# Performance work log

Hardware: AMD Instinct MI355X
Metric: run time of the kernel (lower is better)

## Reference

```python
import jax, jax.numpy as jnp
import numpy as np

DIM = 256
HEADS = 8
WS = 7  # window_size
EPS = 1e-5


def dwconv1d(x, w, b):
    # x: (B, Cg, L); w: (Cg, 1, k); depthwise (groups=Cg), 'same' padding for odd k
    k = w.shape[-1]
    p = k // 2
    y = jax.lax.conv_general_dilated(
        x, w, window_strides=(1,), padding=[(p, p)],
        dimension_numbers=('NCH', 'OIH', 'NCH'),
        feature_group_count=x.shape[1])
    return y + b[None, :, None]


def group_norm(x, scale, bias, groups):
    # x: (B, C, *spatial); normalize over (C//groups, *spatial) per group
    B, C = x.shape[0], x.shape[1]
    xg = x.reshape(B, groups, -1)
    mean = xg.mean(-1, keepdims=True)
    var = xg.var(-1, keepdims=True)
    xn = ((xg - mean) * jax.lax.rsqrt(var + EPS)).reshape(x.shape)
    bshape = (1, C) + (1,) * (x.ndim - 2)
    return xn * scale.reshape(bshape) + bias.reshape(bshape)


def setup_inputs() -> dict:
    key = jax.random.key(0)
    ks = jax.random.split(key, 16)
    gc = DIM // 4
    d = {"x": jax.random.normal(ks[0], (32, DIM, 56, 56), dtype=jnp.float32)}
    for i, k in enumerate([3, 5, 7, 9]):
        d[f"w_dwc{k}"] = jax.random.normal(ks[1 + i], (gc, 1, k), dtype=jnp.float32) * (1.0 / np.sqrt(k))
        d[f"b_dwc{k}"] = jax.random.normal(ks[5 + i], (gc,), dtype=jnp.float32) * 0.02
    d["norm_h_scale"] = jnp.ones((DIM,), jnp.float32)
    d["norm_h_bias"] = jnp.zeros((DIM,), jnp.float32)
    d["norm_w_scale"] = jnp.ones((DIM,), jnp.float32)
    d["norm_w_bias"] = jnp.zeros((DIM,), jnp.float32)
    d["norm_scale"] = jnp.ones((DIM,), jnp.float32)
    d["norm_bias"] = jnp.zeros((DIM,), jnp.float32)
    d["q_w"] = jax.random.normal(ks[9], (DIM,), dtype=jnp.float32)
    d["k_w"] = jax.random.normal(ks[10], (DIM,), dtype=jnp.float32)
    d["v_w"] = jax.random.normal(ks[11], (DIM,), dtype=jnp.float32)
    return d


def reference(x, w_dwc3, b_dwc3, w_dwc5, b_dwc5, w_dwc7, b_dwc7, w_dwc9, b_dwc9,
              norm_h_scale, norm_h_bias, norm_w_scale, norm_w_bias,
              norm_scale, norm_bias, q_w, k_w, v_w):
    b, c, h, w = x.shape
    head_dim = c // HEADS

    def sa_branch(xm, scale, bias):
        # xm: (B, C, L) -> sigmoid(GroupNorm4(concat of 4 depthwise convs))
        p0, p1, p2, p3 = jnp.split(xm, 4, axis=1)
        y = jnp.concatenate([
            dwconv1d(p0, w_dwc3, b_dwc3),
            dwconv1d(p1, w_dwc5, b_dwc5),
            dwconv1d(p2, w_dwc7, b_dwc7),
            dwconv1d(p3, w_dwc9, b_dwc9)], axis=1)
        return jax.nn.sigmoid(group_norm(y, scale, bias, 4))

    x_h_attn = sa_branch(x.mean(axis=3), norm_h_scale, norm_h_bias)[:, :, :, None]  # (B,C,H,1)
    x_w_attn = sa_branch(x.mean(axis=2), norm_w_scale, norm_w_bias)[:, :, None, :]  # (B,C,1,W)
    xg = x * x_h_attn * x_w_attn

    # AvgPool2d(WS, stride=WS)
    hs, ws_ = h // WS, w // WS
    y = xg.reshape(b, c, hs, WS, ws_, WS).mean(axis=(3, 5))  # (B,C,hs,ws)
    y = group_norm(y, norm_scale, norm_bias, 1)

    n = hs * ws_
    q = (y * q_w[None, :, None, None]).reshape(b, HEADS, head_dim, n)
    k = (y * k_w[None, :, None, None]).reshape(b, HEADS, head_dim, n)
    v = (y * v_w[None, :, None, None]).reshape(b, HEADS, head_dim, n)

    attn = jnp.einsum('bhdn,bhen->bhde', q, k) * (head_dim ** -0.5)
    attn = jax.nn.softmax(attn, axis=-1)
    out = jnp.einsum('bhde,bhen->bhdn', attn, v)  # (B,H,hd,n)

    ca = jax.nn.sigmoid(out.reshape(b, c, n).mean(axis=-1))[:, :, None, None]  # (B,C,1,1)
    return ca * xg
```

## Files before the change

kernel.cpp:

```cpp
#include <hip/hip_runtime.h>
#include <cstdint>
#include <cstddef>

#define NB 32
#define NC 256
#define HW 56
#define PLANE (HW*HW)
#define NPLANE (NB*NC)
#define NHEADS 8
#define HDIM 32
#define NPOOL 64
#define EPSV 1e-5f

__global__ __launch_bounds__(256) void k_means(const float* __restrict__ x,
                                               float* __restrict__ hm,
                                               float* __restrict__ wm) {
    int plane = blockIdx.x;
    __shared__ float sm[PLANE];
    const float4* xp = (const float4*)(x + (size_t)plane * PLANE);
    float4* smp = (float4*)sm;
    int t = threadIdx.x;
    for (int f = t; f < PLANE / 4; f += 256) smp[f] = xp[f];
    __syncthreads();
    if (t < 224) {
        int a = t >> 2, q = t & 3;
        float s = 0.f;
#pragma unroll
        for (int i = 0; i < 14; ++i) s += sm[a * 56 + q * 14 + i];
        s += __shfl_xor(s, 1);
        s += __shfl_xor(s, 2);
        if (q == 0) hm[(size_t)plane * 56 + a] = s * (1.f / 56.f);
        float s2 = 0.f;
#pragma unroll
        for (int i = 0; i < 14; ++i) s2 += sm[(q * 14 + i) * 56 + a];
        s2 += __shfl_xor(s2, 1);
        s2 += __shfl_xor(s2, 2);
        if (q == 0) wm[(size_t)plane * 56 + a] = s2 * (1.f / 56.f);
    }
}

__global__ __launch_bounds__(256) void k_branch(
    const float* __restrict__ hm, const float* __restrict__ wm,
    const float* __restrict__ w3, const float* __restrict__ b3,
    const float* __restrict__ w5, const float* __restrict__ b5,
    const float* __restrict__ w7, const float* __restrict__ b7,
    const float* __restrict__ w9, const float* __restrict__ b9,
    const float* __restrict__ hsc, const float* __restrict__ hbi,
    const float* __restrict__ wsc, const float* __restrict__ wbi,
    float* __restrict__ hattn, float* __restrict__ wattn) {
    int mode = blockIdx.x & 1;
    int b = blockIdx.x >> 1;
    const float* src = (mode == 0 ? hm : wm) + (size_t)b * NC * 56;
    const float* scale = (mode == 0 ? hsc : wsc);
    const float* bias = (mode == 0 ? hbi : wbi);
    float* dst = (mode == 0 ? hattn : wattn) + (size_t)b * NC * 56;

    __shared__ float sm[NC * 57];
    int t = threadIdx.x;

    const float4* sp = (const float4*)src;
#pragma unroll
    for (int k = 0; k < 14; ++k) {
        int f = t + 256 * k;
        float4 v = sp[f];
        int c = f / 14, r = f - c * 14;
        float* d = &sm[c * 57 + r * 4];
        d[0] = v.x; d[1] = v.y; d[2] = v.z; d[3] = v.w;
    }
    __syncthreads();

    int c = t;
    int g = c >> 6, cc = c & 63;

    float wc[9];
#pragma unroll
    for (int i = 0; i < 9; ++i) wc[i] = 0.f;
    float bb = 0.f;
    if (g == 0) {
#pragma unroll
        for (int q = 0; q < 3; ++q) wc[3 + q] = w3[cc * 3 + q];
        bb = b3[cc];
    } else if (g == 1) {
#pragma unroll
        for (int q = 0; q < 5; ++q) wc[2 + q] = w5[cc * 5 + q];
        bb = b5[cc];
    } else if (g == 2) {
#pragma unroll
        for (int q = 0; q < 7; ++q) wc[1 + q] = w7[cc * 7 + q];
        bb = b7[cc];
    } else {
#pragma unroll
        for (int q = 0; q < 9; ++q) wc[q] = w9[cc * 9 + q];
        bb = b9[cc];
    }

    float xv[56];
#pragma unroll
    for (int i = 0; i < 56; ++i) xv[i] = sm[c * 57 + i];

    float s1 = 0.f, s2 = 0.f;
#pragma unroll
    for (int i = 0; i < 56; ++i) {
        float a = bb;
#pragma unroll
        for (int d = 0; d < 9; ++d) {
            int j = i + d - 4;
            if (j >= 0 && j < 56) a += wc[d] * xv[j];
        }
        s1 += a;
        s2 += a * a;
    }
#pragma unroll
    for (int off = 32; off >= 1; off >>= 1) {
        s1 += __shfl_xor(s1, off);
        s2 += __shfl_xor(s2, off);
    }
    float mean = s1 * (1.f / 3584.f);
    float var = s2 * (1.f / 3584.f) - mean * mean;
    float rstd = rsqrtf(var + EPSV);
    float scv = scale[c];
    float a_lin = scv * rstd;
    float b_lin = bias[c] - mean * rstd * scv;

#pragma unroll
    for (int i = 0; i < 56; ++i) {
        float a = bb;
#pragma unroll
        for (int d = 0; d < 9; ++d) {
            int j = i + d - 4;
            if (j >= 0 && j < 56) a += wc[d] * xv[j];
        }
        float v = a * a_lin + b_lin;
        sm[c * 57 + i] = 1.f / (1.f + expf(-v));
    }
    __syncthreads();

    float4* dp = (float4*)dst;
#pragma unroll
    for (int k = 0; k < 14; ++k) {
        int f = t + 256 * k;
        int c2 = f / 14, r = f - c2 * 14;
        const float* s = &sm[c2 * 57 + r * 4];
        dp[f] = make_float4(s[0], s[1], s[2], s[3]);
    }
}

__global__ __launch_bounds__(256) void k_pool(const float* __restrict__ x,
                                              const float* __restrict__ hattn,
                                              const float* __restrict__ wattn,
                                              float* __restrict__ ypool) {
    int plane = blockIdx.x;
    __shared__ float sm[PLANE];
    __shared__ float ha[56], wa[56];
    const float4* xp = (const float4*)(x + (size_t)plane * PLANE);
    float4* smp = (float4*)sm;
    int t = threadIdx.x;
    for (int f = t; f < PLANE / 4; f += 256) smp[f] = xp[f];
    if (t < 56) ha[t] = hattn[(size_t)plane * 56 + t];
    else if (t >= 64 && t < 120) wa[t - 64] = wattn[(size_t)plane * 56 + (t - 64)];
    __syncthreads();
    if (t < 64) {
        int i = t >> 3, j = t & 7;
        float s = 0.f;
#pragma unroll
        for (int dh = 0; dh < 7; ++dh) {
            float hv = ha[7 * i + dh];
            float r = 0.f;
#pragma unroll
            for (int dw = 0; dw < 7; ++dw)
                r += sm[(7 * i + dh) * 56 + 7 * j + dw] * wa[7 * j + dw];
            s += hv * r;
        }
        ypool[(size_t)plane * NPOOL + t] = s * (1.f / 49.f);
    }
}

__global__ __launch_bounds__(64) void k_attn(const float* __restrict__ ypool,
                                             const float* __restrict__ nsc,
                                             const float* __restrict__ nbi,
                                             const float* __restrict__ qw,
                                             const float* __restrict__ kw,
                                             const float* __restrict__ vw,
                                             float* __restrict__ ca) {
    int bh = blockIdx.x;
    int b = bh >> 3, h = bh & 7;
    int l = threadIdx.x;

    const float4* bp = (const float4*)(ypool + (size_t)b * NC * NPOOL);
    float s1 = 0.f, s2 = 0.f;
#pragma unroll
    for (int k = 0; k < 64; ++k) {
        float4 v = bp[l + 64 * k];
        s1 += v.x + v.y + v.z + v.w;
        s2 += v.x * v.x + v.y * v.y + v.z * v.z + v.w * v.w;
    }
#pragma unroll
    for (int off = 32; off >= 1; off >>= 1) {
        s1 += __shfl_xor(s1, off);
        s2 += __shfl_xor(s2, off);
    }
    float mean = s1 * (1.f / (NC * NPOOL));
    float var = s2 * (1.f / (NC * NPOOL)) - mean * mean;
    float rstd = rsqrtf(var + EPSV);

    __shared__ float yn[32][65];
    __shared__ float ybar[32];
    __shared__ float G[32][33];
    const float* base = ypool + ((size_t)b * NC + h * HDIM) * NPOOL;
#pragma unroll
    for (int m = 0; m < 32; ++m) {
        int idx = l + 64 * m;
        int d = idx >> 6, p = idx & 63;
        int ch = h * HDIM + d;
        float v = base[idx];
        yn[d][p] = (v - mean) * rstd * nsc[ch] + nbi[ch];
    }
    __syncthreads();
    if (l < 32) {
        float s = 0.f;
#pragma unroll
        for (int p = 0; p < 64; ++p) s += yn[l][p];
        ybar[l] = s * (1.f / 64.f);
    }
    __syncthreads();
#pragma unroll
    for (int m = 0; m < 16; ++m) {
        int idx = l + 64 * m;
        int d = idx >> 5, e = idx & 31;
        float s = 0.f;
#pragma unroll
        for (int p = 0; p < 64; ++p) s += yn[d][p] * yn[e][p];
        G[d][e] = s;
    }
    __syncthreads();
    if (l < 32) {
        int d = l, cd = h * HDIM + d;
        float qs = qw[cd] * 0.17677669529663687f;
        float a[32];
        float mx = -1e30f;
#pragma unroll
        for (int e = 0; e < 32; ++e) {
            a[e] = G[d][e] * qs * kw[h * HDIM + e];
            mx = fmaxf(mx, a[e]);
        }
        float sum = 0.f;
#pragma unroll
        for (int e = 0; e < 32; ++e) {
            a[e] = expf(a[e] - mx);
            sum += a[e];
        }
        float o = 0.f;
#pragma unroll
        for (int e = 0; e < 32; ++e) o += a[e] * vw[h * HDIM + e] * ybar[e];
        o /= sum;
        ca[b * NC + cd] = 1.f / (1.f + expf(-o));
    }
}

__global__ __launch_bounds__(256) void k_final(const float* __restrict__ x,
                                               const float* __restrict__ hattn,
                                               const float* __restrict__ wattn,
                                               const float* __restrict__ ca,
                                               float* __restrict__ out) {
    int plane = blockIdx.x;
    __shared__ float hv[56], wv[56];
    int t = threadIdx.x;
    float cav = ca[plane];
    if (t < 56) hv[t] = hattn[(size_t)plane * 56 + t] * cav;
    else if (t >= 64 && t < 120) wv[t - 64] = wattn[(size_t)plane * 56 + (t - 64)];
    __syncthreads();
    const float4* xp = (const float4*)(x + (size_t)plane * PLANE);
    float4* op = (float4*)(out + (size_t)plane * PLANE);
    for (int f = t; f < PLANE / 4; f += 256) {
        int r = f / 14;
        int s0 = (f - r * 14) * 4;
        float4 v = xp[f];
        float hf = hv[r];
        v.x *= hf * wv[s0];
        v.y *= hf * wv[s0 + 1];
        v.z *= hf * wv[s0 + 2];
        v.w *= hf * wv[s0 + 3];
        op[f] = v;
    }
}

extern "C" void kernel_launch(void* const* d_in, const int* in_sizes, int n_in,
                              void* d_out, int out_size, void* d_ws, size_t ws_size,
                              hipStream_t stream) {
    const float* x   = (const float*)d_in[0];
    const float* w3  = (const float*)d_in[1];
    const float* b3  = (const float*)d_in[2];
    const float* w5  = (const float*)d_in[3];
    const float* b5  = (const float*)d_in[4];
    const float* w7  = (const float*)d_in[5];
    const float* b7  = (const float*)d_in[6];
    const float* w9  = (const float*)d_in[7];
    const float* b9  = (const float*)d_in[8];
    const float* hsc = (const float*)d_in[9];
    const float* hbi = (const float*)d_in[10];
    const float* wsc = (const float*)d_in[11];
    const float* wbi = (const float*)d_in[12];
    const float* nsc = (const float*)d_in[13];
    const float* nbi = (const float*)d_in[14];
    const float* qw  = (const float*)d_in[15];
    const float* kw  = (const float*)d_in[16];
    const float* vw  = (const float*)d_in[17];
    float* out = (float*)d_out;

    float* ws    = (float*)d_ws;
    float* hm    = ws;
    float* wm    = hm + (size_t)NPLANE * 56;
    float* hattn = wm + (size_t)NPLANE * 56;
    float* wattn = hattn + (size_t)NPLANE * 56;
    float* ypool = wattn + (size_t)NPLANE * 56;
    float* cav   = ypool + (size_t)NPLANE * NPOOL;

    k_means<<<NPLANE, 256, 0, stream>>>(x, hm, wm);
    k_branch<<<2 * NB, 256, 0, stream>>>(hm, wm, w3, b3, w5, b5, w7, b7, w9, b9,
                                         hsc, hbi, wsc, wbi, hattn, wattn);
    k_pool<<<NPLANE, 256, 0, stream>>>(x, hattn, wattn, ypool);
    k_attn<<<NB * NHEADS, 64, 0, stream>>>(ypool, nsc, nbi, qw, kw, vw, cav);
    k_final<<<NPLANE, 256, 0, stream>>>(x, hattn, wattn, cav, out);
}
```

Baseline: 285.8 us.

## Fuse all stages into one cooperative persistent kernel with grid syncs

Replaces the five-kernel pipeline (means, conv branch, pooling, attention, final scaling) with a single cooperative kernel of 1024 blocks. Each block handles 8 planes, and the phases are separated by grid-wide barriers. The fused path also spreads the branch stage over 256 blocks split by channel group with templated kernel sizes, and widens the attention stage to 256 threads. This removes launch gaps and the poorly parallel branch kernel, at the cost of grid-sync overhead and serial per-block plane loops. A fallback to the old launches remains if occupancy or the cooperative launch fails.

```diff
diff --git a/kernel.cpp b/kernel.cpp
--- a/kernel.cpp
+++ b/kernel.cpp
@@ -1,6 +1,9 @@
 #include <hip/hip_runtime.h>
+#include <hip/hip_cooperative_groups.h>
 #include <cstdint>
 #include <cstddef>
+
+namespace cg = cooperative_groups;
 
 #define NB 32
 #define NC 256
@@ -11,6 +14,290 @@
 #define HDIM 32
 #define NPOOL 64
 #define EPSV 1e-5f
+#define NBLK 1024
+#define PPB (NPLANE/NBLK)
+#define NUM_CU 256
+
+struct Ph13 { float buf[PLANE]; float ha[56]; float wa[56]; };
+struct Ph2  { float rows[64*57]; float red[8]; };
+struct Ph4  { float yn[32][65]; float G[32][33]; float ybar[32]; float red[8]; float stats[2]; };
+struct Ph5  { float hv[8][56]; float wv[8][56]; };
+union SmemU { Ph13 a; Ph2 b; Ph4 c; Ph5 d; };
+
+template<int K>
+__device__ __forceinline__ void ph2_work(const float* __restrict__ src,
+                                         const float* __restrict__ wk,
+                                         const float* __restrict__ bk,
+                                         const float* __restrict__ scale,
+                                         const float* __restrict__ bias,
+                                         float* __restrict__ dst,
+                                         int cbase, Ph2* S2, int t) {
+    const float4* sp = (const float4*)src;
+#pragma unroll
+    for (int k2 = 0; k2 < 4; ++k2) {
+        int f = t + 256 * k2;
+        if (f < 896) {
+            float4 v = sp[f];
+            int c = f / 14, r = f - c * 14;
+            float* d = &S2->rows[c * 57 + r * 4];
+            d[0] = v.x; d[1] = v.y; d[2] = v.z; d[3] = v.w;
+        }
+    }
+    __syncthreads();
+    int cc = t >> 2, q = t & 3;
+    float w[K];
+#pragma unroll
+    for (int j = 0; j < K; ++j) w[j] = wk[cc * K + j];
+    float bb = bk[cc];
+    const float* row = &S2->rows[cc * 57];
+    float y[14];
+    float s1 = 0.f, s2 = 0.f;
+#pragma unroll
+    for (int il = 0; il < 14; ++il) {
+        int pos = q * 14 + il;
+        float a = bb;
+#pragma unroll
+        for (int j = 0; j < K; ++j) {
+            int p2 = pos + j - K / 2;
+            if (p2 >= 0 && p2 < 56) a += w[j] * row[p2];
+        }
+        y[il] = a; s1 += a; s2 += a * a;
+    }
+#pragma unroll
+    for (int off = 32; off >= 1; off >>= 1) {
+        s1 += __shfl_xor(s1, off);
+        s2 += __shfl_xor(s2, off);
+    }
+    int wv = t >> 6;
+    if ((t & 63) == 0) { S2->red[wv] = s1; S2->red[4 + wv] = s2; }
+    __syncthreads();
+    float t1 = S2->red[0] + S2->red[1] + S2->red[2] + S2->red[3];
+    float t2 = S2->red[4] + S2->red[5] + S2->red[6] + S2->red[7];
+    float mean = t1 * (1.f / 3584.f);
+    float var = t2 * (1.f / 3584.f) - mean * mean;
+    float rstd = rsqrtf(var + EPSV);
+    int c = cbase + cc;
+    float scv = scale[c];
+    float a_lin = scv * rstd, b_lin = bias[c] - mean * rstd * scv;
+#pragma unroll
+    for (int il = 0; il < 14; ++il) {
+        float v = y[il] * a_lin + b_lin;
+        S2->rows[cc * 57 + q * 14 + il] = 1.f / (1.f + expf(-v));
+    }
+    __syncthreads();
+    float4* dp = (float4*)dst;
+#pragma unroll
+    for (int k2 = 0; k2 < 4; ++k2) {
+        int f = t + 256 * k2;
+        if (f < 896) {
+            int c2 = f / 14, r = f - c2 * 14;
+            const float* s = &S2->rows[c2 * 57 + r * 4];
+            dp[f] = make_float4(s[0], s[1], s[2], s[3]);
+        }
+    }
+}
+
+__global__ __launch_bounds__(256, 4) void k_mega(
+    const float* __restrict__ x,
+    const float* __restrict__ w3, const float* __restrict__ b3,
+    const float* __restrict__ w5, const float* __restrict__ b5,
+    const float* __restrict__ w7, const float* __restrict__ b7,
+    const float* __restrict__ w9, const float* __restrict__ b9,
+    const float* __restrict__ hsc, const float* __restrict__ hbi,
+    const float* __restrict__ wsc, const float* __restrict__ wbi,
+    const float* __restrict__ nsc, const float* __restrict__ nbi,
+    const float* __restrict__ qw, const float* __restrict__ kw,
+    const float* __restrict__ vw,
+    float* __restrict__ hm, float* __restrict__ wm,
+    float* __restrict__ hattn, float* __restrict__ wattn,
+    float* __restrict__ ypool, float* __restrict__ ca,
+    float* __restrict__ out)
+{
+    cg::grid_group grid = cg::this_grid();
+    __shared__ SmemU S;
+    const int t = threadIdx.x;
+    const int bid = blockIdx.x;
+
+    for (int p = 0; p < PPB; ++p) {
+        int plane = bid * PPB + p;
+        {
+            const float4* xp = (const float4*)(x + (size_t)plane * PLANE);
+            float4* smp = (float4*)S.a.buf;
+            for (int f = t; f < PLANE / 4; f += 256) smp[f] = xp[f];
+        }
+        __syncthreads();
+        const float* sm = S.a.buf;
+        if (t < 224) {
+            int a = t >> 2, q = t & 3;
+            float s = 0.f;
+#pragma unroll
+            for (int i = 0; i < 14; ++i) s += sm[a * 56 + q * 14 + i];
+            s += __shfl_xor(s, 1); s += __shfl_xor(s, 2);
+            if (q == 0) hm[(size_t)plane * 56 + a] = s * (1.f / 56.f);
+            float s2 = 0.f;
+#pragma unroll
+            for (int i = 0; i < 14; ++i) s2 += sm[(q * 14 + i) * 56 + a];
+            s2 += __shfl_xor(s2, 1); s2 += __shfl_xor(s2, 2);
+            if (q == 0) wm[(size_t)plane * 56 + a] = s2 * (1.f / 56.f);
+        }
+        __syncthreads();
+    }
+    grid.sync();
+
+    if (bid < 256) {
+        int mode = bid & 1, b = (bid >> 1) & 31, g = bid >> 6;
+        const float* src = (mode ? wm : hm) + ((size_t)b * NC + g * 64) * 56;
+        float* dst = (mode ? wattn : hattn) + ((size_t)b * NC + g * 64) * 56;
+        const float* scale = mode ? wsc : hsc;
+        const float* bias = mode ? wbi : hbi;
+        switch (g) {
+            case 0: ph2_work<3>(src, w3, b3, scale, bias, dst, 0,   &S.b, t); break;
+            case 1: ph2_work<5>(src, w5, b5, scale, bias, dst, 64,  &S.b, t); break;
+            case 2: ph2_work<7>(src, w7, b7, scale, bias, dst, 128, &S.b, t); break;
+            default: ph2_work<9>(src, w9, b9, scale, bias, dst, 192, &S.b, t); break;
+        }
+    }
+    grid.sync();
+
+    for (int p = 0; p < PPB; ++p) {
+        int plane = bid * PPB + p;
+        {
+            const float4* xp = (const float4*)(x + (size_t)plane * PLANE);
+            float4* smp = (float4*)S.a.buf;
+            for (int f = t; f < PLANE / 4; f += 256) smp[f] = xp[f];
+            if (t < 56) S.a.ha[t] = hattn[(size_t)plane * 56 + t];
+            else if (t >= 64 && t < 120) S.a.wa[t - 64] = wattn[(size_t)plane * 56 + (t - 64)];
+        }
+        __syncthreads();
+        {
+            const float* sm = S.a.buf;
+            const float* ha = S.a.ha;
+            const float* wa = S.a.wa;
+            int cell = t >> 2, sub = t & 3;
+            int i = cell >> 3, j = cell & 7;
+            float s = 0.f;
+#pragma unroll
+            for (int k2 = 0; k2 < 2; ++k2) {
+                int dh = sub + 4 * k2;
+                if (dh < 7) {
+                    float r = 0.f;
+#pragma unroll
+                    for (int dw = 0; dw < 7; ++dw)
+                        r += sm[(7 * i + dh) * 56 + 7 * j + dw] * wa[7 * j + dw];
+                    s += ha[7 * i + dh] * r;
+                }
+            }
+            s += __shfl_xor(s, 1); s += __shfl_xor(s, 2);
+            if (sub == 0) ypool[(size_t)plane * NPOOL + cell] = s * (1.f / 49.f);
+        }
+        __syncthreads();
+    }
+    grid.sync();
+
+    if (bid < 256) {
+        int b = bid >> 3, h = bid & 7;
+        const float4* bp4 = (const float4*)(ypool + (size_t)b * NC * NPOOL);
+        float s1 = 0.f, s2 = 0.f;
+#pragma unroll
+        for (int k2 = 0; k2 < 16; ++k2) {
+            float4 v = bp4[t + 256 * k2];
+            s1 += v.x + v.y + v.z + v.w;
+            s2 += v.x * v.x + v.y * v.y + v.z * v.z + v.w * v.w;
+        }
+#pragma unroll
+        for (int off = 32; off >= 1; off >>= 1) {
+            s1 += __shfl_xor(s1, off);
+            s2 += __shfl_xor(s2, off);
+        }
+        if ((t & 63) == 0) { S.c.red[t >> 6] = s1; S.c.red[4 + (t >> 6)] = s2; }
+        __syncthreads();
+        if (t == 0) {
+            float t1 = S.c.red[0] + S.c.red[1] + S.c.red[2] + S.c.red[3];
+            float t2 = S.c.red[4] + S.c.red[5] + S.c.red[6] + S.c.red[7];
+            float mean = t1 * (1.f / (NC * NPOOL));
+            float var = t2 * (1.f / (NC * NPOOL)) - mean * mean;
+            S.c.stats[0] = mean; S.c.stats[1] = rsqrtf(var + EPSV);
+        }
+        __syncthreads();
+        float mean = S.c.stats[0], rstd = S.c.stats[1];
+        const float* base = ypool + ((size_t)b * NC + h * HDIM) * NPOOL;
+#pragma unroll
+        for (int m = 0; m < 8; ++m) {
+            int idx = t + 256 * m;
+            int d = idx >> 6, p = idx & 63;
+            int ch = h * HDIM + d;
+            S.c.yn[d][p] = (base[idx] - mean) * rstd * nsc[ch] + nbi[ch];
+        }
+        __syncthreads();
+        if (t < 32) {
+            float s = 0.f;
+#pragma unroll
+            for (int p = 0; p < 64; ++p) s += S.c.yn[t][p];
+            S.c.ybar[t] = s * (1.f / 64.f);
+        }
+        __syncthreads();
+#pragma unroll
+        for (int m = 0; m < 4; ++m) {
+            int idx = t + 256 * m;
+            int d = idx >> 5, e = idx & 31;
+            float s = 0.f;
+#pragma unroll
+            for (int p = 0; p < 64; ++p) s += S.c.yn[d][p] * S.c.yn[e][p];
+            S.c.G[d][e] = s;
+        }
+        __syncthreads();
+        if (t < 32) {
+            int d = t, cd = h * HDIM + d;
+            float qs = qw[cd] * 0.17677669529663687f;
+            float a[32];
+            float mx = -1e30f;
+#pragma unroll
+            for (int e = 0; e < 32; ++e) {
+                a[e] = S.c.G[d][e] * qs * kw[h * HDIM + e];
+                mx = fmaxf(mx, a[e]);
+            }
+            float sum = 0.f;
+#pragma unroll
+            for (int e = 0; e < 32; ++e) {
+                a[e] = expf(a[e] - mx);
+                sum += a[e];
+            }
+            float o = 0.f;
+#pragma unroll
+            for (int e = 0; e < 32; ++e) o += a[e] * vw[h * HDIM + e] * S.c.ybar[e];
+            o /= sum;
+            ca[b * NC + cd] = 1.f / (1.f + expf(-o));
+        }
+    }
+    grid.sync();
+
+    {
+        for (int i = t; i < 448; i += 256) {
+            int p = i / 56, a = i - p * 56;
+            int pl = bid * PPB + p;
+            S.d.hv[p][a] = hattn[(size_t)pl * 56 + a] * ca[pl];
+            S.d.wv[p][a] = wattn[(size_t)pl * 56 + a];
+        }
+        __syncthreads();
+        for (int p = 0; p < PPB; ++p) {
+            int plane = bid * PPB + p;
+            const float* hv = S.d.hv[p];
+            const float* wv = S.d.wv[p];
+            const float4* xp = (const float4*)(x + (size_t)plane * PLANE);
+            float4* op = (float4*)(out + (size_t)plane * PLANE);
+            for (int f = t; f < PLANE / 4; f += 256) {
+                int r = f / 14, s0 = (f - r * 14) * 4;
+                float4 v = xp[f];
+                float hf = hv[r];
+                v.x *= hf * wv[s0];
+                v.y *= hf * wv[s0 + 1];
+                v.z *= hf * wv[s0 + 2];
+                v.w *= hf * wv[s0 + 3];
+                op[f] = v;
+            }
+        }
+    }
+}
 
 __global__ __launch_bounds__(256) void k_means(const float* __restrict__ x,
                                                float* __restrict__ hm,
@@ -27,14 +314,12 @@
         float s = 0.f;
 #pragma unroll
         for (int i = 0; i < 14; ++i) s += sm[a * 56 + q * 14 + i];
-        s += __shfl_xor(s, 1);
-        s += __shfl_xor(s, 2);
+        s += __shfl_xor(s, 1); s += __shfl_xor(s, 2);
         if (q == 0) hm[(size_t)plane * 56 + a] = s * (1.f / 56.f);
         float s2 = 0.f;
 #pragma unroll
         for (int i = 0; i < 14; ++i) s2 += sm[(q * 14 + i) * 56 + a];
-        s2 += __shfl_xor(s2, 1);
-        s2 += __shfl_xor(s2, 2);
+        s2 += __shfl_xor(s2, 1); s2 += __shfl_xor(s2, 2);
         if (q == 0) wm[(size_t)plane * 56 + a] = s2 * (1.f / 56.f);
     }
 }
@@ -57,7 +342,6 @@
 
     __shared__ float sm[NC * 57];
     int t = threadIdx.x;
-
     const float4* sp = (const float4*)src;
 #pragma unroll
     for (int k = 0; k < 14; ++k) {
@@ -71,7 +355,6 @@
 
     int c = t;
     int g = c >> 6, cc = c & 63;
-
     float wc[9];
 #pragma unroll
     for (int i = 0; i < 9; ++i) wc[i] = 0.f;
@@ -121,7 +404,6 @@
     float scv = scale[c];
     float a_lin = scv * rstd;
     float b_lin = bias[c] - mean * rstd * scv;
-
 #pragma unroll
     for (int i = 0; i < 56; ++i) {
         float a = bb;
@@ -134,7 +416,6 @@
         sm[c * 57 + i] = 1.f / (1.f + expf(-v));
     }
     __syncthreads();
-
     float4* dp = (float4*)dst;
 #pragma unroll
     for (int k = 0; k < 14; ++k) {
@@ -185,7 +466,6 @@
     int bh = blockIdx.x;
     int b = bh >> 3, h = bh & 7;
     int l = threadIdx.x;
-
     const float4* bp = (const float4*)(ypool + (size_t)b * NC * NPOOL);
     float s1 = 0.f, s2 = 0.f;
 #pragma unroll
@@ -313,12 +593,34 @@
     float* hattn = wm + (size_t)NPLANE * 56;
     float* wattn = hattn + (size_t)NPLANE * 56;
     float* ypool = wattn + (size_t)NPLANE * 56;
-    float* cav   = ypool + (size_t)NPLANE * NPOOL;
-
-    k_means<<<NPLANE, 256, 0, stream>>>(x, hm, wm);
-    k_branch<<<2 * NB, 256, 0, stream>>>(hm, wm, w3, b3, w5, b5, w7, b7, w9, b9,
-                                         hsc, hbi, wsc, wbi, hattn, wattn);
-    k_pool<<<NPLANE, 256, 0, stream>>>(x, hattn, wattn, ypool);
-    k_attn<<<NB * NHEADS, 64, 0, stream>>>(ypool, nsc, nbi, qw, kw, vw, cav);
-    k_final<<<NPLANE, 256, 0, stream>>>(x, hattn, wattn, cav, out);
-}
+    float* ca    = ypool + (size_t)NPLANE * NPOOL;
+
+    bool coop_done = false;
+    int maxb = 0;
+    hipError_t qe = hipOccupancyMaxActiveBlocksPerMultiprocessor(
+        &maxb, (const void*)k_mega, 256, 0);
+    if (qe == hipSuccess && maxb * NUM_CU >= NBLK) {
+        void* args[] = {
+            (void*)&x,
+            (void*)&w3, (void*)&b3, (void*)&w5, (void*)&b5,
+            (void*)&w7, (void*)&b7, (void*)&w9, (void*)&b9,
+            (void*)&hsc, (void*)&hbi, (void*)&wsc, (void*)&wbi,
+            (void*)&nsc, (void*)&nbi,
+            (void*)&qw, (void*)&kw, (void*)&vw,
+            (void*)&hm, (void*)&wm, (void*)&hattn, (void*)&wattn,
+            (void*)&ypool, (void*)&ca, (void*)&out
+        };
+        hipError_t le = hipLaunchCooperativeKernel((const void*)k_mega, dim3(NBLK),
+                                                   dim3(256), args, 0, stream);
+        coop_done = (le == hipSuccess);
+    }
+    if (!coop_done) {
+        (void)hipGetLastError();
+        k_means<<<NPLANE, 256, 0, stream>>>(x, hm, wm);
+        k_branch<<<2 * NB, 256, 0, stream>>>(hm, wm, w3, b3, w5, b5, w7, b7, w9, b9,
+                                             hsc, hbi, wsc, wbi, hattn, wattn);
+        k_pool<<<NPLANE, 256, 0, stream>>>(x, hattn, wattn, ypool);
+        k_attn<<<NB * NHEADS, 64, 0, stream>>>(ypool, nsc, nbi, qw, kw, vw, ca);
+        k_final<<<NPLANE, 256, 0, stream>>>(x, hattn, wattn, ca, out);
+    }
+}
```

Measured after the change: 284.6 us. About the same (-0.4%).

## Give each wavefront its own plane and prefetch the next plane into registers

Applied to the files above, without the earlier changes.

The three plane-streaming kernels (means, pool, final) now assign one 56x56 plane per wavefront instead of one per 256-thread block. They run a persistent grid of 1024 blocks that loops over planes with a stride of 4096. Means and pool load the next plane into registers while reducing the current one from LDS, and no block-wide barriers are needed. All 64 lanes now do useful work in the reductions, and the row sums use float4 LDS reads. In exchange, LDS use per block is 4 full planes (~50KB) plus 52 float4 registers per lane, which may limit occupancy.

```diff
diff --git a/kernel.cpp b/kernel.cpp
--- a/kernel.cpp
+++ b/kernel.cpp
@@ -15,27 +15,43 @@
 __global__ __launch_bounds__(256) void k_means(const float* __restrict__ x,
                                                float* __restrict__ hm,
                                                float* __restrict__ wm) {
-    int plane = blockIdx.x;
-    __shared__ float sm[PLANE];
-    const float4* xp = (const float4*)(x + (size_t)plane * PLANE);
-    float4* smp = (float4*)sm;
-    int t = threadIdx.x;
-    for (int f = t; f < PLANE / 4; f += 256) smp[f] = xp[f];
-    __syncthreads();
-    if (t < 224) {
-        int a = t >> 2, q = t & 3;
-        float s = 0.f;
-#pragma unroll
-        for (int i = 0; i < 14; ++i) s += sm[a * 56 + q * 14 + i];
-        s += __shfl_xor(s, 1);
-        s += __shfl_xor(s, 2);
-        if (q == 0) hm[(size_t)plane * 56 + a] = s * (1.f / 56.f);
-        float s2 = 0.f;
-#pragma unroll
-        for (int i = 0; i < 14; ++i) s2 += sm[(q * 14 + i) * 56 + a];
-        s2 += __shfl_xor(s2, 1);
-        s2 += __shfl_xor(s2, 2);
-        if (q == 0) wm[(size_t)plane * 56 + a] = s2 * (1.f / 56.f);
+    __shared__ float sm[4][PLANE];
+    const int wid = threadIdx.x >> 6, lane = threadIdx.x & 63;
+    float* myL = sm[wid];
+    float4* myL4 = (float4*)myL;
+    const int gw = blockIdx.x * 4 + wid;
+    float4 buf[13];
+
+    {
+        const float4* pb = (const float4*)(x + (size_t)gw * PLANE);
+#pragma unroll
+        for (int k = 0; k < 12; ++k) buf[k] = pb[k * 64 + lane];
+        if (lane < 16) buf[12] = pb[768 + lane];
+    }
+    for (int plane = gw; plane < NPLANE; plane += 4096) {
+#pragma unroll
+        for (int k = 0; k < 12; ++k) myL4[k * 64 + lane] = buf[k];
+        if (lane < 16) myL4[768 + lane] = buf[12];
+        int np = plane + 4096;
+        if (np < NPLANE) {
+            const float4* pb = (const float4*)(x + (size_t)np * PLANE);
+#pragma unroll
+            for (int k = 0; k < 12; ++k) buf[k] = pb[k * 64 + lane];
+            if (lane < 16) buf[12] = pb[768 + lane];
+        }
+        if (lane < 56) {
+            float s = 0.f;
+#pragma unroll
+            for (int i = 0; i < 14; ++i) {
+                float4 v = myL4[lane * 14 + i];
+                s += (v.x + v.y) + (v.z + v.w);
+            }
+            hm[(size_t)plane * 56 + lane] = s * (1.f / 56.f);
+            float s2 = 0.f;
+#pragma unroll
+            for (int r = 0; r < 56; ++r) s2 += myL[r * 56 + lane];
+            wm[(size_t)plane * 56 + lane] = s2 * (1.f / 56.f);
+        }
     }
 }
 
@@ -57,7 +73,6 @@
 
     __shared__ float sm[NC * 57];
     int t = threadIdx.x;
-
     const float4* sp = (const float4*)src;
 #pragma unroll
     for (int k = 0; k < 14; ++k) {
@@ -71,7 +86,6 @@
 
     int c = t;
     int g = c >> 6, cc = c & 63;
-
     float wc[9];
 #pragma unroll
     for (int i = 0; i < 9; ++i) wc[i] = 0.f;
@@ -121,7 +135,6 @@
     float scv = scale[c];
     float a_lin = scv * rstd;
     float b_lin = bias[c] - mean * rstd * scv;
-
 #pragma unroll
     for (int i = 0; i < 56; ++i) {
         float a = bb;
@@ -134,7 +147,6 @@
         sm[c * 57 + i] = 1.f / (1.f + expf(-v));
     }
     __syncthreads();
-
     float4* dp = (float4*)dst;
 #pragma unroll
     for (int k = 0; k < 14; ++k) {
@@ -149,29 +161,51 @@
                                               const float* __restrict__ hattn,
                                               const float* __restrict__ wattn,
                                               float* __restrict__ ypool) {
-    int plane = blockIdx.x;
-    __shared__ float sm[PLANE];
-    __shared__ float ha[56], wa[56];
-    const float4* xp = (const float4*)(x + (size_t)plane * PLANE);
-    float4* smp = (float4*)sm;
-    int t = threadIdx.x;
-    for (int f = t; f < PLANE / 4; f += 256) smp[f] = xp[f];
-    if (t < 56) ha[t] = hattn[(size_t)plane * 56 + t];
-    else if (t >= 64 && t < 120) wa[t - 64] = wattn[(size_t)plane * 56 + (t - 64)];
-    __syncthreads();
-    if (t < 64) {
-        int i = t >> 3, j = t & 7;
-        float s = 0.f;
-#pragma unroll
-        for (int dh = 0; dh < 7; ++dh) {
-            float hv = ha[7 * i + dh];
-            float r = 0.f;
-#pragma unroll
-            for (int dw = 0; dw < 7; ++dw)
-                r += sm[(7 * i + dh) * 56 + 7 * j + dw] * wa[7 * j + dw];
-            s += hv * r;
-        }
-        ypool[(size_t)plane * NPOOL + t] = s * (1.f / 49.f);
+    __shared__ float sm[4][PLANE];
+    __shared__ float gg[4][112];
+    const int wid = threadIdx.x >> 6, lane = threadIdx.x & 63;
+    float* myL = sm[wid];
+    float4* myL4 = (float4*)myL;
+    float* myG = gg[wid];
+    const int gw = blockIdx.x * 4 + wid;
+    float4 buf[13];
+    float gh, gwv;
+
+    {
+        const float4* pb = (const float4*)(x + (size_t)gw * PLANE);
+#pragma unroll
+        for (int k = 0; k < 12; ++k) buf[k] = pb[k * 64 + lane];
+        if (lane < 16) buf[12] = pb[768 + lane];
+        gh = (lane < 56) ? hattn[(size_t)gw * 56 + lane] : 0.f;
+        gwv = (lane < 56) ? wattn[(size_t)gw * 56 + lane] : 0.f;
+    }
+    for (int plane = gw; plane < NPLANE; plane += 4096) {
+#pragma unroll
+        for (int k = 0; k < 12; ++k) myL4[k * 64 + lane] = buf[k];
+        if (lane < 16) myL4[768 + lane] = buf[12];
+        if (lane < 56) { myG[lane] = gh; myG[56 + lane] = gwv; }
+        int np = plane + 4096;
+        if (np < NPLANE) {
+            const float4* pb = (const float4*)(x + (size_t)np * PLANE);
+#pragma unroll
+            for (int k = 0; k < 12; ++k) buf[k] = pb[k * 64 + lane];
+            if (lane < 16) buf[12] = pb[768 + lane];
+            gh = (lane < 56) ? hattn[(size_t)np * 56 + lane] : 0.f;
+            gwv = (lane < 56) ? wattn[(size_t)np * 56 + lane] : 0.f;
+        }
+        {
+            int i = lane >> 3, j = lane & 7;
+            float s = 0.f;
+#pragma unroll
+            for (int dh = 0; dh < 7; ++dh) {
+                float r = 0.f;
+#pragma unroll
+                for (int dw = 0; dw < 7; ++dw)
+                    r += myL[(7 * i + dh) * 56 + 7 * j + dw] * myG[56 + 7 * j + dw];
+                s += myG[7 * i + dh] * r;
+            }
+            ypool[(size_t)plane * NPOOL + lane] = s * (1.f / 49.f);
+        }
     }
 }
 
@@ -185,7 +219,6 @@
     int bh = blockIdx.x;
     int b = bh >> 3, h = bh & 7;
     int l = threadIdx.x;
-
     const float4* bp = (const float4*)(ypool + (size_t)b * NC * NPOOL);
     float s1 = 0.f, s2 = 0.f;
 #pragma unroll
@@ -262,25 +295,45 @@
                                                const float* __restrict__ wattn,
                                                const float* __restrict__ ca,
                                                float* __restrict__ out) {
-    int plane = blockIdx.x;
-    __shared__ float hv[56], wv[56];
-    int t = threadIdx.x;
-    float cav = ca[plane];
-    if (t < 56) hv[t] = hattn[(size_t)plane * 56 + t] * cav;
-    else if (t >= 64 && t < 120) wv[t - 64] = wattn[(size_t)plane * 56 + (t - 64)];
-    __syncthreads();
-    const float4* xp = (const float4*)(x + (size_t)plane * PLANE);
-    float4* op = (float4*)(out + (size_t)plane * PLANE);
-    for (int f = t; f < PLANE / 4; f += 256) {
-        int r = f / 14;
-        int s0 = (f - r * 14) * 4;
-        float4 v = xp[f];
-        float hf = hv[r];
-        v.x *= hf * wv[s0];
-        v.y *= hf * wv[s0 + 1];
-        v.z *= hf * wv[s0 + 2];
-        v.w *= hf * wv[s0 + 3];
-        op[f] = v;
+    __shared__ float gg[4][128];
+    const int wid = threadIdx.x >> 6, lane = threadIdx.x & 63;
+    float* myG = gg[wid];
+    const int gw = blockIdx.x * 4 + wid;
+
+    for (int plane = gw; plane < NPLANE; plane += 4096) {
+        if (lane < 56) {
+            myG[lane] = hattn[(size_t)plane * 56 + lane] * ca[plane];
+            myG[64 + lane] = wattn[(size_t)plane * 56 + lane];
+        }
+        const float4* xp = (const float4*)(x + (size_t)plane * PLANE);
+        float4* op = (float4*)(out + (size_t)plane * PLANE);
+        float4 buf[13];
+#pragma unroll
+        for (int k = 0; k < 12; ++k) buf[k] = xp[k * 64 + lane];
+        if (lane < 16) buf[12] = xp[768 + lane];
+#pragma unroll
+        for (int k = 0; k < 12; ++k) {
+            int f = k * 64 + lane;
+            int r = f / 14, s0 = (f - r * 14) * 4;
+            float hf = myG[r];
+            float4 v = buf[k];
+            v.x *= hf * myG[64 + s0];
+            v.y *= hf * myG[64 + s0 + 1];
+            v.z *= hf * myG[64 + s0 + 2];
+            v.w *= hf * myG[64 + s0 + 3];
+            op[f] = v;
+        }
+        if (lane < 16) {
+            int f = 768 + lane;
+            int r = f / 14, s0 = (f - r * 14) * 4;
+            float hf = myG[r];
+            float4 v = buf[12];
+            v.x *= hf * myG[64 + s0];
+            v.y *= hf * myG[64 + s0 + 1];
+            v.z *= hf * myG[64 + s0 + 2];
+            v.w *= hf * myG[64 + s0 + 3];
+            op[f] = v;
+        }
     }
 }
 
@@ -313,12 +366,12 @@
     float* hattn = wm + (size_t)NPLANE * 56;
     float* wattn = hattn + (size_t)NPLANE * 56;
     float* ypool = wattn + (size_t)NPLANE * 56;
-    float* cav   = ypool + (size_t)NPLANE * NPOOL;
-
-    k_means<<<NPLANE, 256, 0, stream>>>(x, hm, wm);
+    float* ca    = ypool + (size_t)NPLANE * NPOOL;
+
+    k_means<<<1024, 256, 0, stream>>>(x, hm, wm);
     k_branch<<<2 * NB, 256, 0, stream>>>(hm, wm, w3, b3, w5, b5, w7, b7, w9, b9,
                                          hsc, hbi, wsc, wbi, hattn, wattn);
-    k_pool<<<NPLANE, 256, 0, stream>>>(x, hattn, wattn, ypool);
-    k_attn<<<NB * NHEADS, 64, 0, stream>>>(ypool, nsc, nbi, qw, kw, vw, cav);
-    k_final<<<NPLANE, 256, 0, stream>>>(x, hattn, wattn, cav, out);
-}
+    k_pool<<<1024, 256, 0, stream>>>(x, hattn, wattn, ypool);
+    k_attn<<<NB * NHEADS, 64, 0, stream>>>(ypool, nsc, nbi, qw, kw, vw, ca);
+    k_final<<<1024, 256, 0, stream>>>(x, hattn, wattn, ca, out);
+}
```

Result: slower. 335.1 us (+17.3%).
